# Kernel tuning notes

Hardware: AMD Instinct MI355X
Metric: run time of the kernel (lower is better)

The kernel has to match this reference:

```python
import jax, jax.numpy as jnp
import numpy as np


def _rope(v, pos, head_dim):
    # v: [H, D]; rotate consecutive pairs by angle pos * theta_j
    theta = 1.0 / (10000.0 ** (jnp.arange(0, head_dim, 2, dtype=jnp.float32) / head_dim))
    ang = pos * theta                      # [D/2]
    cos, sin = jnp.cos(ang), jnp.sin(ang)
    vr = v.reshape(v.shape[0], -1, 2)      # [H, D/2, 2]
    re = vr[..., 0] * cos - vr[..., 1] * sin
    im = vr[..., 0] * sin + vr[..., 1] * cos
    return jnp.stack([re, im], axis=-1).reshape(v.shape)


def setup_inputs() -> dict:
    key = jax.random.key(0)
    ks = jax.random.split(key, 7)
    dim, H, D, S = 4096, 32, 128, 2048
    scale = 0.02
    return {
        "x": jax.random.normal(ks[0], (dim,), dtype=jnp.float32),
        "wq": jax.random.normal(ks[1], (dim, dim), dtype=jnp.float32) * scale,
        "wk": jax.random.normal(ks[2], (dim, dim), dtype=jnp.float32) * scale,
        "wv": jax.random.normal(ks[3], (dim, dim), dtype=jnp.float32) * scale,
        "wo": jax.random.normal(ks[4], (dim, dim), dtype=jnp.float32) * scale,
        "cache_k": jax.random.normal(ks[5], (S, H, D), dtype=jnp.float32),
        "cache_v": jax.random.normal(ks[6], (S, H, D), dtype=jnp.float32),
        "pos": 1536,
    }


def reference(x, wq, wk, wv, wo, cache_k, cache_v, pos):
    H, D = cache_k.shape[1], cache_k.shape[2]
    # nn.Linear without bias: y = W @ x
    xq = (wq @ x).reshape(H, D)
    xk = (wk @ x).reshape(H, D)
    xv = (wv @ x).reshape(H, D)
    xq = _rope(xq, pos, D)
    xk = _rope(xk, pos, D)
    # KV cache append (pos is a static Python int)
    cache_k = cache_k.at[pos].set(xk)
    cache_v = cache_v.at[pos].set(xv)
    keys = cache_k[: pos + 1]              # [P, H, D]
    values = cache_v[: pos + 1]            # [P, H, D]
    # single-query decode attention per head
    scores = jnp.einsum("hd,phd->hp", xq, keys) / jnp.sqrt(jnp.float32(D))
    scores = jax.nn.softmax(scores, axis=-1)
    out = jnp.einsum("hp,phd->hd", scores, values)   # [H, D]
    return wo @ out.reshape(-1)
```

## Files before the change

kernel.cpp:

```cpp
#include <hip/hip_runtime.h>
#include <math.h>

#define DIM 4096
#define H 32
#define D 128
#define SMAX 2048
#define CHUNK 32
#define NCHUNK (SMAX / CHUNK)
#define PART_STRIDE 130

typedef float v4f __attribute__((ext_vector_type(4)));

__device__ __forceinline__ void load_half(v4f (&buf)[8], const float* __restrict__ wp, int off) {
#pragma unroll
    for (int i = 0; i < 8; ++i)
        buf[i] = *reinterpret_cast<const v4f*>(wp + i * 256 + off);
}

template <int XO>
__device__ __forceinline__ float dot_half(const v4f (&buf)[8], const v4f (&xr)[16]) {
    float s0 = 0.f, s1 = 0.f, s2 = 0.f, s3 = 0.f;
#pragma unroll
    for (int i = 0; i < 8; ++i) {
        s0 = fmaf(buf[i].x, xr[XO + i].x, s0);
        s1 = fmaf(buf[i].y, xr[XO + i].y, s1);
        s2 = fmaf(buf[i].z, xr[XO + i].z, s2);
        s3 = fmaf(buf[i].w, xr[XO + i].w, s3);
    }
    return (s0 + s1) + (s2 + s3);
}

__device__ __forceinline__ float wave_sum(float v) {
#pragma unroll
    for (int o = 32; o; o >>= 1) v += __shfl_xor(v, o);
    return v;
}

#define SB() __builtin_amdgcn_sched_barrier(0)

__global__ void __launch_bounds__(256) qkv_rope(
        const float* __restrict__ wq, const float* __restrict__ wk,
        const float* __restrict__ wv, const float* __restrict__ x,
        const int* __restrict__ pos_p,
        float* __restrict__ xq, float* __restrict__ xk, float* __restrict__ xv) {
    int t = threadIdx.x, lane = t & 63;
    int W = blockIdx.x * 4 + (t >> 6);
    int r0 = W * 2;
    int off = lane * 4;

    v4f xr[16];
#pragma unroll
    for (int i = 0; i < 16; ++i)
        xr[i] = *reinterpret_cast<const v4f*>(x + i * 256 + off);

    const float* q0 = wq + (size_t)r0 * DIM;
    const float* k0 = wk + (size_t)r0 * DIM;
    const float* v0 = wv + (size_t)r0 * DIM;

    v4f A[8], B[8];
    float dq0, dq1, dk0, dk1, dv0, dv1;

    load_half(A, q0, off);
    load_half(B, q0 + 2048, off);            SB();
    dq0  = dot_half<0>(A, xr);
    load_half(A, q0 + DIM, off);             SB();
    dq0 += dot_half<8>(B, xr);
    load_half(B, q0 + DIM + 2048, off);      SB();
    dq1  = dot_half<0>(A, xr);
    load_half(A, k0, off);                   SB();
    dq1 += dot_half<8>(B, xr);
    load_half(B, k0 + 2048, off);            SB();
    dk0  = dot_half<0>(A, xr);
    load_half(A, k0 + DIM, off);             SB();
    dk0 += dot_half<8>(B, xr);
    load_half(B, k0 + DIM + 2048, off);      SB();
    dk1  = dot_half<0>(A, xr);
    load_half(A, v0, off);                   SB();
    dk1 += dot_half<8>(B, xr);
    load_half(B, v0 + 2048, off);            SB();
    dv0  = dot_half<0>(A, xr);
    load_half(A, v0 + DIM, off);             SB();
    dv0 += dot_half<8>(B, xr);
    load_half(B, v0 + DIM + 2048, off);      SB();
    dv1  = dot_half<0>(A, xr);
    dv1 += dot_half<8>(B, xr);

    dq0 = wave_sum(dq0); dq1 = wave_sum(dq1);
    dk0 = wave_sum(dk0); dk1 = wave_sum(dk1);
    dv0 = wave_sum(dv0); dv1 = wave_sum(dv1);

    if (lane == 0) {
        int pos = *pos_p;
        int j = W & 63;
        float theta = powf(10000.0f, -(float)(2 * j) / (float)D);
        float ang = (float)pos * theta;
        float s, c;
        sincosf(ang, &s, &c);
        xq[r0]     = dq0 * c - dq1 * s;
        xq[r0 + 1] = dq0 * s + dq1 * c;
        xk[r0]     = dk0 * c - dk1 * s;
        xk[r0 + 1] = dk0 * s + dk1 * c;
        xv[r0]     = dv0;
        xv[r0 + 1] = dv1;
    }
}

__global__ void __launch_bounds__(256) matvec_o(
        const float* __restrict__ w_, const float* __restrict__ vin,
        float* __restrict__ y) {
    int t = threadIdx.x, lane = t & 63;
    int W = blockIdx.x * 4 + (t >> 6);
    int r0 = W * 2;
    int off = lane * 4;

    v4f xr[16];
#pragma unroll
    for (int i = 0; i < 16; ++i)
        xr[i] = *reinterpret_cast<const v4f*>(vin + i * 256 + off);

    const float* w0 = w_ + (size_t)r0 * DIM;

    v4f A[8], B[8];
    float d0, d1;
    load_half(A, w0, off);
    load_half(B, w0 + 2048, off);            SB();
    d0  = dot_half<0>(A, xr);
    load_half(A, w0 + DIM, off);             SB();
    d0 += dot_half<8>(B, xr);
    load_half(B, w0 + DIM + 2048, off);      SB();
    d1  = dot_half<0>(A, xr);
    d1 += dot_half<8>(B, xr);

    d0 = wave_sum(d0); d1 = wave_sum(d1);
    if (lane == 0) { y[r0] = d0; y[r0 + 1] = d1; }
}

__global__ void attn_partial(const float* __restrict__ cache_k, const float* __restrict__ cache_v,
                             const float* __restrict__ xq, const float* __restrict__ xk,
                             const float* __restrict__ xv, const int* __restrict__ pos_p,
                             float* __restrict__ partials) {
    __shared__ float lds_m[4], lds_l[4];
    __shared__ float lds_acc[4][128];
    int h = blockIdx.x;
    int c = blockIdx.y;
    int lane = threadIdx.x;
    int g  = lane >> 4;
    int gl = lane & 15;
    int pos = *pos_p;
    int base = c * CHUNK;
    int p1 = min(base + CHUNK, pos + 1);
    float* pp = partials + (size_t)(h * NCHUNK + c) * PART_STRIDE;

    if (base > pos) {
        if (lane == 0) { pp[0] = -INFINITY; pp[1] = 0.f; }
        reinterpret_cast<float2*>(pp + 2)[lane] = make_float2(0.f, 0.f);
        return;
    }

    const float4* qv = reinterpret_cast<const float4*>(xq + h * D + gl * 8);
    const float4 q0 = qv[0], q1 = qv[1];

    float m = -INFINITY, l = 0.f;
    float4 acc0 = make_float4(0.f, 0.f, 0.f, 0.f);
    float4 acc1 = make_float4(0.f, 0.f, 0.f, 0.f);

    for (int p = base + g; p < p1; p += 4) {
        const float* kp = (p == pos) ? (xk + h * D)
                                     : (cache_k + ((size_t)p * H + h) * D);
        const float4* kv4 = reinterpret_cast<const float4*>(kp + gl * 8);
        float4 k0 = kv4[0], k1 = kv4[1];
        float d = q0.x * k0.x + q0.y * k0.y + q0.z * k0.z + q0.w * k0.w
                + q1.x * k1.x + q1.y * k1.y + q1.z * k1.z + q1.w * k1.w;
        d += __shfl_xor(d, 1);
        d += __shfl_xor(d, 2);
        d += __shfl_xor(d, 4);
        d += __shfl_xor(d, 8);
        float s = d * 0.08838834764831845f;
        float mn = fmaxf(m, s);
        float corr = __expf(m - mn);
        float wgt  = __expf(s - mn);
        const float* vp = (p == pos) ? (xv + h * D)
                                     : (cache_v + ((size_t)p * H + h) * D);
        const float4* vv4 = reinterpret_cast<const float4*>(vp + gl * 8);
        float4 v0 = vv4[0], v1 = vv4[1];
        l = l * corr + wgt;
        acc0.x = fmaf(wgt, v0.x, acc0.x * corr);
        acc0.y = fmaf(wgt, v0.y, acc0.y * corr);
        acc0.z = fmaf(wgt, v0.z, acc0.z * corr);
        acc0.w = fmaf(wgt, v0.w, acc0.w * corr);
        acc1.x = fmaf(wgt, v1.x, acc1.x * corr);
        acc1.y = fmaf(wgt, v1.y, acc1.y * corr);
        acc1.z = fmaf(wgt, v1.z, acc1.z * corr);
        acc1.w = fmaf(wgt, v1.w, acc1.w * corr);
        m = mn;
    }

    if (gl == 0) { lds_m[g] = m; lds_l[g] = l; }
    *reinterpret_cast<float4*>(&lds_acc[g][gl * 8])     = acc0;
    *reinterpret_cast<float4*>(&lds_acc[g][gl * 8 + 4]) = acc1;
    __syncthreads();
    float M = fmaxf(fmaxf(lds_m[0], lds_m[1]), fmaxf(lds_m[2], lds_m[3]));
    float w0 = __expf(lds_m[0] - M);
    float w1 = __expf(lds_m[1] - M);
    float w2 = __expf(lds_m[2] - M);
    float w3 = __expf(lds_m[3] - M);
    float L  = w0 * lds_l[0] + w1 * lds_l[1] + w2 * lds_l[2] + w3 * lds_l[3];
    int d0 = 2 * lane;
    float s0 = w0 * lds_acc[0][d0]     + w1 * lds_acc[1][d0]
             + w2 * lds_acc[2][d0]     + w3 * lds_acc[3][d0];
    float s1 = w0 * lds_acc[0][d0 + 1] + w1 * lds_acc[1][d0 + 1]
             + w2 * lds_acc[2][d0 + 1] + w3 * lds_acc[3][d0 + 1];
    if (lane == 0) { pp[0] = M; pp[1] = L; }
    reinterpret_cast<float2*>(pp + 2)[lane] = make_float2(s0, s1);
}

__global__ void attn_combine(const float* __restrict__ partials, float* __restrict__ out_attn) {
    int h = blockIdx.x;
    int lane = threadIdx.x;
    float m = -INFINITY;
    for (int c = 0; c < NCHUNK; ++c)
        m = fmaxf(m, partials[(size_t)(h * NCHUNK + c) * PART_STRIDE]);
    float L = 0.f, a0 = 0.f, a1 = 0.f;
    for (int c = 0; c < NCHUNK; ++c) {
        const float* pp = partials + (size_t)(h * NCHUNK + c) * PART_STRIDE;
        float w = __expf(pp[0] - m);
        L += pp[1] * w;
        float2 a = reinterpret_cast<const float2*>(pp + 2)[lane];
        a0 += w * a.x;
        a1 += w * a.y;
    }
    float inv = 1.f / L;
    out_attn[h * D + 2 * lane]     = a0 * inv;
    out_attn[h * D + 2 * lane + 1] = a1 * inv;
}

extern "C" void kernel_launch(void* const* d_in, const int* in_sizes, int n_in,
                              void* d_out, int out_size, void* d_ws, size_t ws_size,
                              hipStream_t stream) {
    const float* x       = (const float*)d_in[0];
    const float* wq      = (const float*)d_in[1];
    const float* wk      = (const float*)d_in[2];
    const float* wv      = (const float*)d_in[3];
    const float* wo      = (const float*)d_in[4];
    const float* cache_k = (const float*)d_in[5];
    const float* cache_v = (const float*)d_in[6];
    const int*   pos     = (const int*)d_in[7];

    float* ws       = (float*)d_ws;
    float* xq       = ws;
    float* xk       = ws + DIM;
    float* xv       = ws + 2 * DIM;
    float* partials = ws + 3 * DIM;
    float* out_attn = partials + H * NCHUNK * PART_STRIDE;
    float* out      = (float*)d_out;

    qkv_rope<<<512, 256, 0, stream>>>(wq, wk, wv, x, pos, xq, xk, xv);
    attn_partial<<<dim3(H, NCHUNK), 64, 0, stream>>>(cache_k, cache_v, xq, xk, xv, pos, partials);
    attn_combine<<<H, 64, 0, stream>>>(partials, out_attn);
    matvec_o<<<512, 256, 0, stream>>>(wo, out_attn, out);
}
```

Before: 82.72 us.

## Split QKV projection into block-per-row-pair QK RoPE kernel and separate V matvec

Replaces the fused QKV kernel, where each wave handled two rows of all three matrices, with two kernels. The QK kernel has a whole 256-thread block reduce each row pair, with a grid-stride loop over Q and K pairs and a double-buffered shared-memory reduction. The V kernel uses one block per row. The aim is more parallelism and shorter per-wave dependency chains when streaming the weights, at the cost of an extra kernel launch, more block syncs and reductions, and losing the software-pipelined loads.

```diff
diff --git a/kernel.cpp b/kernel.cpp
--- a/kernel.cpp
+++ b/kernel.cpp
@@ -11,6 +11,94 @@
 
 typedef float v4f __attribute__((ext_vector_type(4)));
 
+__device__ __forceinline__ float wave_sum(float v) {
+#pragma unroll
+    for (int o = 32; o; o >>= 1) v += __shfl_xor(v, o);
+    return v;
+}
+
+__global__ void __launch_bounds__(256) qk_rope(
+        const float* __restrict__ wq, const float* __restrict__ wk,
+        const float* __restrict__ x, const int* __restrict__ pos_p,
+        float* __restrict__ xq, float* __restrict__ xk) {
+    __shared__ float red[2][2][4];
+    int t = threadIdx.x, lane = t & 63, wv_ = t >> 6;
+    int pos = *pos_p;
+
+    v4f xr[4];
+#pragma unroll
+    for (int i = 0; i < 4; ++i)
+        xr[i] = *reinterpret_cast<const v4f*>(x + i * 1024 + t * 4);
+
+    int par = 0;
+    for (int tp = blockIdx.x; tp < 4096; tp += gridDim.x, par ^= 1) {
+        bool isq = tp < 2048;
+        int pr = isq ? tp : tp - 2048;
+        const float* base = (isq ? wq : wk) + (size_t)pr * 2 * DIM;
+
+        v4f wa[4], wb[4];
+#pragma unroll
+        for (int i = 0; i < 4; ++i) {
+            wa[i] = *reinterpret_cast<const v4f*>(base + i * 1024 + t * 4);
+            wb[i] = *reinterpret_cast<const v4f*>(base + DIM + i * 1024 + t * 4);
+        }
+        float a0 = 0.f, a1 = 0.f, a2 = 0.f, a3 = 0.f;
+        float b0 = 0.f, b1 = 0.f, b2 = 0.f, b3 = 0.f;
+#pragma unroll
+        for (int i = 0; i < 4; ++i) {
+            a0 = fmaf(wa[i].x, xr[i].x, a0);
+            a1 = fmaf(wa[i].y, xr[i].y, a1);
+            a2 = fmaf(wa[i].z, xr[i].z, a2);
+            a3 = fmaf(wa[i].w, xr[i].w, a3);
+            b0 = fmaf(wb[i].x, xr[i].x, b0);
+            b1 = fmaf(wb[i].y, xr[i].y, b1);
+            b2 = fmaf(wb[i].z, xr[i].z, b2);
+            b3 = fmaf(wb[i].w, xr[i].w, b3);
+        }
+        float da = wave_sum((a0 + a1) + (a2 + a3));
+        float db = wave_sum((b0 + b1) + (b2 + b3));
+        if (lane == 0) { red[par][0][wv_] = da; red[par][1][wv_] = db; }
+        __syncthreads();
+        if (t == 0) {
+            float d0 = red[par][0][0] + red[par][0][1] + red[par][0][2] + red[par][0][3];
+            float d1 = red[par][1][0] + red[par][1][1] + red[par][1][2] + red[par][1][3];
+            int j = pr & 63;
+            float theta = powf(10000.0f, -(float)(2 * j) / (float)D);
+            float ang = (float)pos * theta;
+            float s, c;
+            sincosf(ang, &s, &c);
+            float* o = isq ? xq : xk;
+            o[2 * pr]     = d0 * c - d1 * s;
+            o[2 * pr + 1] = d0 * s + d1 * c;
+        }
+    }
+}
+
+__global__ void __launch_bounds__(256) v_mat(
+        const float* __restrict__ wv, const float* __restrict__ x,
+        float* __restrict__ xv) {
+    __shared__ float red[4];
+    int row = blockIdx.x;
+    const float* w = wv + (size_t)row * DIM;
+    int t = threadIdx.x;
+    float acc = 0.f;
+#pragma unroll
+    for (int i = 0; i < 4; ++i) {
+        int idx = (i * 256 + t) * 4;
+        const float4 a = *reinterpret_cast<const float4*>(w + idx);
+        const float4 b = *reinterpret_cast<const float4*>(x + idx);
+        acc = fmaf(a.x, b.x, acc);
+        acc = fmaf(a.y, b.y, acc);
+        acc = fmaf(a.z, b.z, acc);
+        acc = fmaf(a.w, b.w, acc);
+    }
+#pragma unroll
+    for (int off = 32; off; off >>= 1) acc += __shfl_xor(acc, off);
+    if ((t & 63) == 0) red[t >> 6] = acc;
+    __syncthreads();
+    if (t == 0) xv[row] = red[0] + red[1] + red[2] + red[3];
+}
+
 __device__ __forceinline__ void load_half(v4f (&buf)[8], const float* __restrict__ wp, int off) {
 #pragma unroll
     for (int i = 0; i < 8; ++i)
@@ -30,80 +118,7 @@
     return (s0 + s1) + (s2 + s3);
 }
 
-__device__ __forceinline__ float wave_sum(float v) {
-#pragma unroll
-    for (int o = 32; o; o >>= 1) v += __shfl_xor(v, o);
-    return v;
-}
-
 #define SB() __builtin_amdgcn_sched_barrier(0)
-
-__global__ void __launch_bounds__(256) qkv_rope(
-        const float* __restrict__ wq, const float* __restrict__ wk,
-        const float* __restrict__ wv, const float* __restrict__ x,
-        const int* __restrict__ pos_p,
-        float* __restrict__ xq, float* __restrict__ xk, float* __restrict__ xv) {
-    int t = threadIdx.x, lane = t & 63;
-    int W = blockIdx.x * 4 + (t >> 6);
-    int r0 = W * 2;
-    int off = lane * 4;
-
-    v4f xr[16];
-#pragma unroll
-    for (int i = 0; i < 16; ++i)
-        xr[i] = *reinterpret_cast<const v4f*>(x + i * 256 + off);
-
-    const float* q0 = wq + (size_t)r0 * DIM;
-    const float* k0 = wk + (size_t)r0 * DIM;
-    const float* v0 = wv + (size_t)r0 * DIM;
-
-    v4f A[8], B[8];
-    float dq0, dq1, dk0, dk1, dv0, dv1;
-
-    load_half(A, q0, off);
-    load_half(B, q0 + 2048, off);            SB();
-    dq0  = dot_half<0>(A, xr);
-    load_half(A, q0 + DIM, off);             SB();
-    dq0 += dot_half<8>(B, xr);
-    load_half(B, q0 + DIM + 2048, off);      SB();
-    dq1  = dot_half<0>(A, xr);
-    load_half(A, k0, off);                   SB();
-    dq1 += dot_half<8>(B, xr);
-    load_half(B, k0 + 2048, off);            SB();
-    dk0  = dot_half<0>(A, xr);
-    load_half(A, k0 + DIM, off);             SB();
-    dk0 += dot_half<8>(B, xr);
-    load_half(B, k0 + DIM + 2048, off);      SB();
-    dk1  = dot_half<0>(A, xr);
-    load_half(A, v0, off);                   SB();
-    dk1 += dot_half<8>(B, xr);
-    load_half(B, v0 + 2048, off);            SB();
-    dv0  = dot_half<0>(A, xr);
-    load_half(A, v0 + DIM, off);             SB();
-    dv0 += dot_half<8>(B, xr);
-    load_half(B, v0 + DIM + 2048, off);      SB();
-    dv1  = dot_half<0>(A, xr);
-    dv1 += dot_half<8>(B, xr);
-
-    dq0 = wave_sum(dq0); dq1 = wave_sum(dq1);
-    dk0 = wave_sum(dk0); dk1 = wave_sum(dk1);
-    dv0 = wave_sum(dv0); dv1 = wave_sum(dv1);
-
-    if (lane == 0) {
-        int pos = *pos_p;
-        int j = W & 63;
-        float theta = powf(10000.0f, -(float)(2 * j) / (float)D);
-        float ang = (float)pos * theta;
-        float s, c;
-        sincosf(ang, &s, &c);
-        xq[r0]     = dq0 * c - dq1 * s;
-        xq[r0 + 1] = dq0 * s + dq1 * c;
-        xk[r0]     = dk0 * c - dk1 * s;
-        xk[r0 + 1] = dk0 * s + dk1 * c;
-        xv[r0]     = dv0;
-        xv[r0 + 1] = dv1;
-    }
-}
 
 __global__ void __launch_bounds__(256) matvec_o(
         const float* __restrict__ w_, const float* __restrict__ vin,
@@ -119,7 +134,6 @@
         xr[i] = *reinterpret_cast<const v4f*>(vin + i * 256 + off);
 
     const float* w0 = w_ + (size_t)r0 * DIM;
-
     v4f A[8], B[8];
     float d0, d1;
     load_half(A, w0, off);
@@ -254,7 +268,8 @@
     float* out_attn = partials + H * NCHUNK * PART_STRIDE;
     float* out      = (float*)d_out;
 
-    qkv_rope<<<512, 256, 0, stream>>>(wq, wk, wv, x, pos, xq, xk, xv);
+    qk_rope<<<2048, 256, 0, stream>>>(wq, wk, x, pos, xq, xk);
+    v_mat<<<DIM, 256, 0, stream>>>(wv, x, xv);
     attn_partial<<<dim3(H, NCHUNK), 64, 0, stream>>>(cache_k, cache_v, xq, xk, xv, pos, partials);
     attn_combine<<<H, 64, 0, stream>>>(partials, out_attn);
     matvec_o<<<512, 256, 0, stream>>>(wo, out_attn, out);
```

New measurement: 80.47 us. -2.7%, faster.
